# Optimization experiments

Measured on AMD Instinct MI355X. Metric: run time of the kernel, lower is better.

## Reference

```python
import jax, jax.numpy as jnp
import numpy as np

MARGIN = 1.0

def _pairwise_sqdist(z):
    # ||zi - zj||^2 = ||zi||^2 + ||zj||^2 - 2 zi.zj
    sq = jnp.sum(z * z, axis=-1)  # [N]
    d2 = sq[:, None] + sq[None, :] - 2.0 * (z @ z.T)
    return jnp.maximum(d2, 0.0)

def _safe_sqrt(d2):
    # sqrt with well-defined gradient at 0 (matches cdist values; diag = 0)
    pos = d2 > 0.0
    return jnp.where(pos, jnp.sqrt(jnp.where(pos, d2, 1.0)), 0.0)

def setup_inputs() -> dict:
    key = jax.random.key(0)
    k1, k2 = jax.random.split(key)
    z = jax.random.normal(k1, (8192, 128), dtype=jnp.float32)
    labels = jax.random.randint(k2, (8192,), 0, 100, dtype=jnp.int64)
    return {"z": z, "labels": labels}

def reference(z, labels):
    d2 = _pairwise_sqdist(z)              # [N, N] squared distances
    dist = _safe_sqrt(d2)                 # [N, N] distances
    label_eq = labels[:, None] == labels[None, :]
    pos = jnp.where(label_eq, d2, 0.0)
    neg = jnp.where(label_eq, 0.0, jnp.square(jax.nn.relu(MARGIN - dist)))
    return jnp.mean(pos + neg)
```

## Files before the change

### kernel.cpp

```cpp
#include <hip/hip_runtime.h>
#include <stdint.h>


#define NROWS 8192
#define DIMK  128
#define NB    64
#define NBLK  (NB * (NB + 1) / 2)

typedef __attribute__((ext_vector_type(4))) float f32x4;

#define AS_GLOBAL __attribute__((address_space(1)))
#define AS_LDS    __attribute__((address_space(3)))

__global__ __launch_bounds__(256) void prep_kernel(
    const float* __restrict__ z, unsigned char* __restrict__ zb,
    float* __restrict__ sq) {
  int tid = threadIdx.x;
  int row = (blockIdx.x << 3) + (tid >> 5);
  int c32 = tid & 31;
  float4 x = ((const float4*)(z + (size_t)row * DIMK))[c32];
  int u = __builtin_amdgcn_cvt_pk_fp8_f32(x.x, x.y, 0, false);
  u     = __builtin_amdgcn_cvt_pk_fp8_f32(x.z, x.w, u, true);
  float r0 = __builtin_amdgcn_cvt_f32_fp8(u, 0);
  float r1 = __builtin_amdgcn_cvt_f32_fp8(u, 1);
  float r2 = __builtin_amdgcn_cvt_f32_fp8(u, 2);
  float r3 = __builtin_amdgcn_cvt_f32_fp8(u, 3);
  float s = (r0 * r0 + r1 * r1) + (r2 * r2 + r3 * r3);
  int k0 = c32 << 2;
  int g  = (((k0 >> 3) & 3) << 2) | (k0 >> 5);
  int p  = ((g ^ (row & 15)) << 3) + (k0 & 7);
  *(uint32_t*)(zb + (size_t)row * DIMK + p) = (uint32_t)u;
  #pragma unroll
  for (int off = 16; off; off >>= 1) s += __shfl_down(s, off, 32);
  if (c32 == 0) sq[row] = s;
}

__global__ __launch_bounds__(512, 6) void loss_kernel(
    const unsigned char* __restrict__ zb, const float* __restrict__ sq,
    const int* __restrict__ labels, float* __restrict__ partials) {
  __shared__ __align__(16) unsigned char ldsA[16384];
  __shared__ __align__(16) unsigned char ldsB[16384];
  __shared__ __align__(16) float sqAl[128];
  __shared__ __align__(16) float sqBl[128];
  __shared__ __align__(16) int   laAl[128];
  __shared__ __align__(16) int   laBl[128];
  __shared__ float red[8];

  int tid = threadIdx.x, lane = tid & 63, wave = tid >> 6;

  int bid = blockIdx.x;
  #define TRI(rr) ((rr) * NB - ((rr) * ((rr) - 1)) / 2)
  int r = (int)(((float)(2 * NB + 1) -
                 sqrtf((float)((2 * NB + 1) * (2 * NB + 1) - 8 * bid))) * 0.5f);
  if (r < 0) r = 0; if (r > NB - 1) r = NB - 1;
  while (TRI(r + 1) <= bid) ++r;
  while (TRI(r) > bid) --r;
  int bi = r, bj = bid - TRI(r) + r;

  const unsigned char* Ab = zb + (((size_t)bi << 7) * DIMK);
  const unsigned char* Bb = zb + (((size_t)bj << 7) * DIMK);
  #pragma unroll
  for (int t = 0; t < 2; ++t) {
    int L0 = (t << 9) + (wave << 6);
    int L  = L0 + lane;
    __builtin_amdgcn_global_load_lds(
        (const AS_GLOBAL void*)(uintptr_t)(Ab + (size_t)L * 16),
        (AS_LDS void*)(uintptr_t)(ldsA + (size_t)L0 * 16), 16, 0, 0);
    __builtin_amdgcn_global_load_lds(
        (const AS_GLOBAL void*)(uintptr_t)(Bb + (size_t)L * 16),
        (AS_LDS void*)(uintptr_t)(ldsB + (size_t)L0 * 16), 16, 0, 0);
  }
  if (tid < 128) {
    sqAl[tid] = sq[(bi << 7) + tid];
    laAl[tid] = labels[(bi << 7) + tid];
  } else if (tid < 256) {
    int t2 = tid & 127;
    sqBl[t2] = sq[(bj << 7) + t2];
    laBl[t2] = labels[(bj << 7) + t2];
  }
  asm volatile("s_waitcnt vmcnt(0)" ::: "memory");
  __syncthreads();

  int wm = wave >> 1, wn = wave & 1;
  int lc = lane & 15;
  int q  = lane >> 4;
  f32x4 acc[2][4] = {};
  #pragma unroll
  for (int ks = 0; ks < 4; ++ks) {
    int so = ((((q << 2) | ks) ^ lc) << 3);
    long a0 = *(const long*)(ldsA + ((wm << 5)      + lc) * 128 + so);
    long a1 = *(const long*)(ldsA + ((wm << 5) + 16 + lc) * 128 + so);
    long b0 = *(const long*)(ldsB + ((wn << 6)      + lc) * 128 + so);
    long b1 = *(const long*)(ldsB + ((wn << 6) + 16 + lc) * 128 + so);
    long b2 = *(const long*)(ldsB + ((wn << 6) + 32 + lc) * 128 + so);
    long b3 = *(const long*)(ldsB + ((wn << 6) + 48 + lc) * 128 + so);
    acc[0][0] = __builtin_amdgcn_mfma_f32_16x16x32_fp8_fp8(a0, b0, acc[0][0], 0, 0, 0);
    acc[0][1] = __builtin_amdgcn_mfma_f32_16x16x32_fp8_fp8(a0, b1, acc[0][1], 0, 0, 0);
    acc[0][2] = __builtin_amdgcn_mfma_f32_16x16x32_fp8_fp8(a0, b2, acc[0][2], 0, 0, 0);
    acc[0][3] = __builtin_amdgcn_mfma_f32_16x16x32_fp8_fp8(a0, b3, acc[0][3], 0, 0, 0);
    acc[1][0] = __builtin_amdgcn_mfma_f32_16x16x32_fp8_fp8(a1, b0, acc[1][0], 0, 0, 0);
    acc[1][1] = __builtin_amdgcn_mfma_f32_16x16x32_fp8_fp8(a1, b1, acc[1][1], 0, 0, 0);
    acc[1][2] = __builtin_amdgcn_mfma_f32_16x16x32_fp8_fp8(a1, b2, acc[1][2], 0, 0, 0);
    acc[1][3] = __builtin_amdgcn_mfma_f32_16x16x32_fp8_fp8(a1, b3, acc[1][3], 0, 0, 0);
  }

  int r0 = q << 2;
  float sn_[4]; int ln_[4];
  #pragma unroll
  for (int j = 0; j < 4; ++j) {
    int n = (wn << 6) + (j << 4) + lc;
    sn_[j] = sqBl[n]; ln_[j] = laBl[n];
  }
  float ps0 = 0.f, ps1 = 0.f, ps2 = 0.f, ps3 = 0.f;
  float mnall = 1e30f;
  #pragma unroll
  for (int i = 0; i < 2; ++i) {
    int mb = (wm << 5) + (i << 4) + r0;
    f32x4 sm4 = *(const f32x4*)&sqAl[mb];
    int4  lm4 = *(const int4*)&laAl[mb];
    #pragma unroll
    for (int j = 0; j < 4; ++j) {
      float d0  = fmaf(-2.f, acc[i][j][0], sm4[0] + sn_[j]);
      float d1  = fmaf(-2.f, acc[i][j][1], sm4[1] + sn_[j]);
      float d2_ = fmaf(-2.f, acc[i][j][2], sm4[2] + sn_[j]);
      float d3  = fmaf(-2.f, acc[i][j][3], sm4[3] + sn_[j]);
      mnall = fminf(mnall, fminf(fminf(d0, d1), fminf(d2_, d3)));
      ps0 += (lm4.x == ln_[j]) ? d0  : 0.f;
      ps1 += (lm4.y == ln_[j]) ? d1  : 0.f;
      ps2 += (lm4.z == ln_[j]) ? d2_ : 0.f;
      ps3 += (lm4.w == ln_[j]) ? d3  : 0.f;
    }
  }
  if (__builtin_expect(__any(mnall < 1.f), 0)) {
    ps0 = ps1 = ps2 = ps3 = 0.f;
    #pragma unroll
    for (int i = 0; i < 2; ++i) {
      int mb = (wm << 5) + (i << 4) + r0;
      f32x4 sm4 = *(const f32x4*)&sqAl[mb];
      int4  lm4 = *(const int4*)&laAl[mb];
      #pragma unroll
      for (int j = 0; j < 4; ++j) {
        float dc, t;
        dc = fmaxf(fmaf(-2.f, acc[i][j][0], sm4[0] + sn_[j]), 0.f);
        t = fmaxf(1.f - sqrtf(dc), 0.f);
        ps0 += (lm4.x == ln_[j]) ? dc : t * t;
        dc = fmaxf(fmaf(-2.f, acc[i][j][1], sm4[1] + sn_[j]), 0.f);
        t = fmaxf(1.f - sqrtf(dc), 0.f);
        ps1 += (lm4.y == ln_[j]) ? dc : t * t;
        dc = fmaxf(fmaf(-2.f, acc[i][j][2], sm4[2] + sn_[j]), 0.f);
        t = fmaxf(1.f - sqrtf(dc), 0.f);
        ps2 += (lm4.z == ln_[j]) ? dc : t * t;
        dc = fmaxf(fmaf(-2.f, acc[i][j][3], sm4[3] + sn_[j]), 0.f);
        t = fmaxf(1.f - sqrtf(dc), 0.f);
        ps3 += (lm4.w == ln_[j]) ? dc : t * t;
      }
    }
  }
  float psum = (ps0 + ps1) + (ps2 + ps3);
  float w = (bi == bj) ? 1.f : 2.f;
  psum *= w * (1.f / (8192.f * 8192.f));

  #pragma unroll
  for (int off = 32; off; off >>= 1) psum += __shfl_down(psum, off);
  if (lane == 0) red[wave] = psum;
  __syncthreads();
  if (tid == 0) {
    float s = 0.f;
    #pragma unroll
    for (int k = 0; k < 8; ++k) s += red[k];
    partials[bid] = s;
  }
}

__global__ __launch_bounds__(256) void reduce_kernel(
    const float* __restrict__ partials, float* __restrict__ out) {
  int tid = threadIdx.x, lane = tid & 63, wave = tid >> 6;
  float s = 0.f;
  for (int k = tid; k < NBLK; k += 256) s += partials[k];
  #pragma unroll
  for (int off = 32; off; off >>= 1) s += __shfl_down(s, off);
  __shared__ float red[4];
  if (lane == 0) red[wave] = s;
  __syncthreads();
  if (tid == 0) out[0] = red[0] + red[1] + red[2] + red[3];
}

extern "C" void kernel_launch(void* const* d_in, const int* in_sizes, int n_in,
                              void* d_out, int out_size, void* d_ws, size_t ws_size,
                              hipStream_t stream) {
  const float* z      = (const float*)d_in[0];
  const int*   labels = (const int*)d_in[1];
  float*       out    = (float*)d_out;
  unsigned char* zb   = (unsigned char*)d_ws;
  char* p = (char*)d_ws + (size_t)NROWS * DIMK;
  float* sq       = (float*)p;
  float* partials = (float*)(p + NROWS * 4);

  prep_kernel<<<NROWS / 8, 256, 0, stream>>>(z, zb, sq);
  loss_kernel<<<NBLK, 512, 0, stream>>>(zb, sq, labels, partials);
  reduce_kernel<<<1, 256, 0, stream>>>(partials, out);
}
```

Baseline: 73.85 us.

## Split each 128x128 pair tile into two 64-row blocks of 256 threads

Each triangular block pair is now handled by two blocks, each computing half the rows with 4 waves instead of 8. This doubles the grid and cuts LDS per block, aiming for better occupancy and tail balance across CUs. In exchange, the B tile and its metadata are loaded twice per pair, which increases L2 traffic, and the number of partials doubles.

```diff
diff --git a/kernel.cpp b/kernel.cpp
--- a/kernel.cpp
+++ b/kernel.cpp
@@ -5,7 +5,8 @@
 #define NROWS 8192
 #define DIMK  128
 #define NB    64
-#define NBLK  (NB * (NB + 1) / 2)
+#define NPAIR (NB * (NB + 1) / 2)
+#define NBLK  (NPAIR * 2)
 
 typedef __attribute__((ext_vector_type(4))) float f32x4;
 
@@ -35,48 +36,54 @@
   if (c32 == 0) sq[row] = s;
 }
 
-__global__ __launch_bounds__(512, 6) void loss_kernel(
+__global__ __launch_bounds__(256, 6) void loss_kernel(
     const unsigned char* __restrict__ zb, const float* __restrict__ sq,
     const int* __restrict__ labels, float* __restrict__ partials) {
-  __shared__ __align__(16) unsigned char ldsA[16384];
+  __shared__ __align__(16) unsigned char ldsA[8192];
   __shared__ __align__(16) unsigned char ldsB[16384];
-  __shared__ __align__(16) float sqAl[128];
+  __shared__ __align__(16) float sqAl[64];
   __shared__ __align__(16) float sqBl[128];
-  __shared__ __align__(16) int   laAl[128];
+  __shared__ __align__(16) int   laAl[64];
   __shared__ __align__(16) int   laBl[128];
-  __shared__ float red[8];
+  __shared__ float red[4];
 
   int tid = threadIdx.x, lane = tid & 63, wave = tid >> 6;
 
   int bid = blockIdx.x;
+  int t = bid >> 1, h = bid & 1;
   #define TRI(rr) ((rr) * NB - ((rr) * ((rr) - 1)) / 2)
   int r = (int)(((float)(2 * NB + 1) -
-                 sqrtf((float)((2 * NB + 1) * (2 * NB + 1) - 8 * bid))) * 0.5f);
+                 sqrtf((float)((2 * NB + 1) * (2 * NB + 1) - 8 * t))) * 0.5f);
   if (r < 0) r = 0; if (r > NB - 1) r = NB - 1;
-  while (TRI(r + 1) <= bid) ++r;
-  while (TRI(r) > bid) --r;
-  int bi = r, bj = bid - TRI(r) + r;
-
-  const unsigned char* Ab = zb + (((size_t)bi << 7) * DIMK);
-  const unsigned char* Bb = zb + (((size_t)bj << 7) * DIMK);
-  #pragma unroll
-  for (int t = 0; t < 2; ++t) {
-    int L0 = (t << 9) + (wave << 6);
-    int L  = L0 + lane;
+  while (TRI(r + 1) <= t) ++r;
+  while (TRI(r) > t) --r;
+  int bi = r, bj = t - TRI(r) + r;
+  int row0 = (bi << 7) + (h << 6);
+  int col0 = (bj << 7);
+
+  const unsigned char* Ab = zb + (size_t)row0 * DIMK;
+  const unsigned char* Bb = zb + (size_t)col0 * DIMK;
+  #pragma unroll
+  for (int it = 0; it < 2; ++it) {
+    int L0 = (it << 8) + (wave << 6);
     __builtin_amdgcn_global_load_lds(
-        (const AS_GLOBAL void*)(uintptr_t)(Ab + (size_t)L * 16),
+        (const AS_GLOBAL void*)(uintptr_t)(Ab + (size_t)(L0 + lane) * 16),
         (AS_LDS void*)(uintptr_t)(ldsA + (size_t)L0 * 16), 16, 0, 0);
+  }
+  #pragma unroll
+  for (int it = 0; it < 4; ++it) {
+    int L0 = (it << 8) + (wave << 6);
     __builtin_amdgcn_global_load_lds(
-        (const AS_GLOBAL void*)(uintptr_t)(Bb + (size_t)L * 16),
+        (const AS_GLOBAL void*)(uintptr_t)(Bb + (size_t)(L0 + lane) * 16),
         (AS_LDS void*)(uintptr_t)(ldsB + (size_t)L0 * 16), 16, 0, 0);
   }
-  if (tid < 128) {
-    sqAl[tid] = sq[(bi << 7) + tid];
-    laAl[tid] = labels[(bi << 7) + tid];
-  } else if (tid < 256) {
-    int t2 = tid & 127;
-    sqBl[t2] = sq[(bj << 7) + t2];
-    laBl[t2] = labels[(bj << 7) + t2];
+  if (tid < 64) {
+    sqAl[tid] = sq[row0 + tid];
+    laAl[tid] = labels[row0 + tid];
+  } else if (tid < 192) {
+    int t2 = tid - 64;
+    sqBl[t2] = sq[col0 + t2];
+    laBl[t2] = labels[col0 + t2];
   }
   asm volatile("s_waitcnt vmcnt(0)" ::: "memory");
   __syncthreads();
@@ -140,19 +147,19 @@
       int4  lm4 = *(const int4*)&laAl[mb];
       #pragma unroll
       for (int j = 0; j < 4; ++j) {
-        float dc, t;
+        float dc, tt;
         dc = fmaxf(fmaf(-2.f, acc[i][j][0], sm4[0] + sn_[j]), 0.f);
-        t = fmaxf(1.f - sqrtf(dc), 0.f);
-        ps0 += (lm4.x == ln_[j]) ? dc : t * t;
+        tt = fmaxf(1.f - sqrtf(dc), 0.f);
+        ps0 += (lm4.x == ln_[j]) ? dc : tt * tt;
         dc = fmaxf(fmaf(-2.f, acc[i][j][1], sm4[1] + sn_[j]), 0.f);
-        t = fmaxf(1.f - sqrtf(dc), 0.f);
-        ps1 += (lm4.y == ln_[j]) ? dc : t * t;
+        tt = fmaxf(1.f - sqrtf(dc), 0.f);
+        ps1 += (lm4.y == ln_[j]) ? dc : tt * tt;
         dc = fmaxf(fmaf(-2.f, acc[i][j][2], sm4[2] + sn_[j]), 0.f);
-        t = fmaxf(1.f - sqrtf(dc), 0.f);
-        ps2 += (lm4.z == ln_[j]) ? dc : t * t;
+        tt = fmaxf(1.f - sqrtf(dc), 0.f);
+        ps2 += (lm4.z == ln_[j]) ? dc : tt * tt;
         dc = fmaxf(fmaf(-2.f, acc[i][j][3], sm4[3] + sn_[j]), 0.f);
-        t = fmaxf(1.f - sqrtf(dc), 0.f);
-        ps3 += (lm4.w == ln_[j]) ? dc : t * t;
+        tt = fmaxf(1.f - sqrtf(dc), 0.f);
+        ps3 += (lm4.w == ln_[j]) ? dc : tt * tt;
       }
     }
   }
@@ -164,12 +171,8 @@
   for (int off = 32; off; off >>= 1) psum += __shfl_down(psum, off);
   if (lane == 0) red[wave] = psum;
   __syncthreads();
-  if (tid == 0) {
-    float s = 0.f;
-    #pragma unroll
-    for (int k = 0; k < 8; ++k) s += red[k];
-    partials[bid] = s;
-  }
+  if (tid == 0)
+    partials[bid] = (red[0] + red[1]) + (red[2] + red[3]);
 }
 
 __global__ __launch_bounds__(256) void reduce_kernel(
@@ -197,6 +200,6 @@
   float* partials = (float*)(p + NROWS * 4);
 
   prep_kernel<<<NROWS / 8, 256, 0, stream>>>(z, zb, sq);
-  loss_kernel<<<NBLK, 512, 0, stream>>>(zb, sq, labels, partials);
+  loss_kernel<<<NBLK, 256, 0, stream>>>(zb, sq, labels, partials);
   reduce_kernel<<<1, 256, 0, stream>>>(partials, out);
 }
```

New measurement: 78.02 us. 5.6% more time.
